# Kernel optimization log

Measured on AMD Instinct MI355X. Metric: run time of the kernel, lower is better.

Reference implementation:

```python
import jax, jax.numpy as jnp
import numpy as np

B, K, D = 256, 256, 3          # graphs, destroy sets per graph, destroy size
N_PER = 55                      # nodes per graph (from Linear(55+3, 1))
N = B * N_PER                   # total batched nodes
E = N * 8                       # edges, avg degree 8
EMB = 64


def setup_inputs() -> dict:
    key = jax.random.key(0)
    ks = jax.random.split(key, 16)
    inp = {
        'coords': jax.random.uniform(ks[0], (N, 2), dtype=jnp.float32),
        'src': jax.random.randint(ks[1], (E,), 0, N, dtype=jnp.int32),
        'dst': jax.random.randint(ks[2], (E,), 0, N, dtype=jnp.int32),
        'destroy_ids': jax.random.randint(ks[3], (B, K, D), 0, N_PER, dtype=jnp.int32),
        'W_embed': jax.random.normal(ks[4], (2, EMB), dtype=jnp.float32) * 0.5,
        'b_embed': jax.random.normal(ks[5], (EMB,), dtype=jnp.float32) * 0.1,
        'Wself': jax.random.normal(ks[6], (3, EMB, EMB), dtype=jnp.float32) * (1.0 / np.sqrt(EMB)),
        'Wneigh': jax.random.normal(ks[7], (3, EMB, EMB), dtype=jnp.float32) * (1.0 / np.sqrt(EMB)) * 0.1,
        'gnn_b': jax.random.normal(ks[8], (3, EMB), dtype=jnp.float32) * 0.1,
        'W1': jax.random.normal(ks[9], (EMB, 32), dtype=jnp.float32) * (1.0 / np.sqrt(EMB)),
        'b1': jax.random.normal(ks[10], (32,), dtype=jnp.float32) * 0.1,
        'W2': jax.random.normal(ks[11], (32, 32), dtype=jnp.float32) * (1.0 / np.sqrt(32)),
        'b2': jax.random.normal(ks[12], (32,), dtype=jnp.float32) * 0.1,
        'W3': jax.random.normal(ks[13], (32, 1), dtype=jnp.float32) * (1.0 / np.sqrt(32)),
        'b3': jax.random.normal(ks[14], (1,), dtype=jnp.float32) * 0.1,
        'Wp': jax.random.normal(ks[15], (N_PER + D, 1), dtype=jnp.float32) * (1.0 / np.sqrt(N_PER + D)),
        'bp': jnp.zeros((1,), dtype=jnp.float32),
    }
    return inp


def reference(coords, src, dst, destroy_ids, W_embed, b_embed, Wself, Wneigh,
              gnn_b, W1, b1, W2, b2, W3, b3, Wp, bp):
    lrelu = lambda x: jax.nn.leaky_relu(x, 0.01)
    # node coord embedding: [N, 64]
    h = coords @ W_embed + b_embed
    # residual message passing (GNN), 3 layers
    for l in range(Wself.shape[0]):
        agg = jax.ops.segment_sum(h[src], dst, num_segments=N)  # irregular gather/scatter
        h = jax.nn.relu(h @ Wself[l] + agg @ Wneigh[l] + gnn_b[l]) + h
    g_embed = h.reshape(B, N_PER, EMB)                 # [B, 55, 64]
    # vectorized replacement of the per-id .item() gather loops
    coords_b = coords.reshape(B, N_PER, 2)
    d_coords = jax.vmap(lambda c, idx: c[idx])(coords_b, destroy_ids)  # [B, K, 3, 2]
    d_embed = d_coords @ W_embed + b_embed             # [B, K, 3, 64]
    # concat graph embedding with each destroy-set embedding along node dim
    g_b = jnp.broadcast_to(g_embed[:, None], (B, K, N_PER, EMB))
    final = jnp.concatenate([g_b, d_embed], axis=2)    # [B, K, 58, 64]
    # MLP: 64->32->32->1 then pred over node dim 58->1
    x = lrelu(final @ W1 + b1)
    x = lrelu(x @ W2 + b2)
    x = (x @ W3 + b3)[..., 0]                          # [B, K, 58]
    out = (x @ Wp + bp)[..., 0]                        # [B, K]
    return out
```

## Files before the change

kernel.cpp:

```cpp
#include <hip/hip_runtime.h>
#include <hip/hip_bf16.h>

constexpr int NB   = 256;
constexpr int KK   = 256;
constexpr int NPER = 55;
constexpr int NN   = NB * NPER;
constexpr int EMB  = 64;
constexpr int CAP  = 32;
constexpr int NT   = 512;

using ull = unsigned long long;
__device__ __forceinline__ void st_f1(float* p, float x) {
  union { float f; unsigned u; } v; v.f = x;
  __hip_atomic_store((unsigned*)p, v.u, __ATOMIC_RELAXED, __HIP_MEMORY_SCOPE_AGENT);
}
__device__ __forceinline__ void st_f2(float* p, float x, float y) {
  union { float f[2]; ull u; } v; v.f[0] = x; v.f[1] = y;
  __hip_atomic_store((ull*)p, v.u, __ATOMIC_RELAXED, __HIP_MEMORY_SCOPE_AGENT);
}
__device__ __forceinline__ float2 ld_f2(const float* p) {
  union { ull u; float f[2]; } v;
  v.u = __hip_atomic_load((const ull*)p, __ATOMIC_RELAXED, __HIP_MEMORY_SCOPE_AGENT);
  return make_float2(v.f[0], v.f[1]);
}
__device__ __forceinline__ int ld_i1(const int* p) {
  return __hip_atomic_load(p, __ATOMIC_RELAXED, __HIP_MEMORY_SCOPE_AGENT);
}
__device__ __forceinline__ void st_i1(int* p, int x) {
  __hip_atomic_store(p, x, __ATOMIC_RELAXED, __HIP_MEMORY_SCOPE_AGENT);
}
__device__ __forceinline__ int2 ld_i2(const int* p) {
  union { ull u; int i[2]; } v;
  v.u = __hip_atomic_load((const ull*)p, __ATOMIC_RELAXED, __HIP_MEMORY_SCOPE_AGENT);
  return make_int2(v.i[0], v.i[1]);
}

constexpr int ZERO_N = NN + NB + 16;
__global__ __launch_bounds__(256) void init_kernel(int* __restrict__ p) {
  int i = blockIdx.x * 256 + threadIdx.x;
  if (i < ZERO_N) p[i] = 0;
}

__device__ __forceinline__ void grid_barrier(int* arr, int* flag, int ep) {
  __syncthreads();
  int tid = threadIdx.x;
  if (blockIdx.x == 0) {
    if (tid == 0) st_i1(&arr[0], ep);
    if (tid < NB) {
      while (ld_i1(&arr[tid]) < ep) __builtin_amdgcn_s_sleep(8);
    }
    __syncthreads();
    if (tid == 0) st_i1(flag, ep);
  } else {
    if (tid == 0) {
      st_i1(&arr[blockIdx.x], ep);
      while (ld_i1(flag) < ep) __builtin_amdgcn_s_sleep(8);
    }
  }
  __syncthreads();
}

__device__ __forceinline__ float mlp_lds(const float (&x)[64],
    const float* sW1, const float* sW2, const float* sW3,
    const float* sb1, const float* sb2, float b3v) {
  float a[32];
#pragma unroll
  for (int j = 0; j < 32; j++) a[j] = sb1[j];
#pragma unroll
  for (int i = 0; i < 64; i++) {
    float xi = x[i];
#pragma unroll
    for (int j = 0; j < 32; j++) a[j] = fmaf(xi, sW1[i * 32 + j], a[j]);
  }
#pragma unroll
  for (int j = 0; j < 32; j++) a[j] = (a[j] >= 0.f) ? a[j] : 0.01f * a[j];
  float c[32];
#pragma unroll
  for (int j = 0; j < 32; j++) c[j] = sb2[j];
#pragma unroll
  for (int i = 0; i < 32; i++) {
    float ai = a[i];
#pragma unroll
    for (int j = 0; j < 32; j++) c[j] = fmaf(ai, sW2[i * 32 + j], c[j]);
  }
#pragma unroll
  for (int j = 0; j < 32; j++) c[j] = (c[j] >= 0.f) ? c[j] : 0.01f * c[j];
  float r = b3v;
#pragma unroll
  for (int i = 0; i < 32; i++) r = fmaf(c[i], sW3[i], r);
  return r;
}

__global__ __launch_bounds__(NT) void mega_kernel(
    const float* __restrict__ coords, const int* __restrict__ src,
    const int* __restrict__ dst, const int* __restrict__ ids,
    const float* __restrict__ We, const float* __restrict__ be,
    const float* __restrict__ Wself, const float* __restrict__ Wneigh,
    const float* __restrict__ gnnb,
    const float* __restrict__ W1, const float* __restrict__ b1,
    const float* __restrict__ W2, const float* __restrict__ b2,
    const float* __restrict__ W3, const float* __restrict__ b3,
    const float* __restrict__ Wp, const float* __restrict__ bp,
    float* __restrict__ h0, float* __restrict__ h1,
    int* __restrict__ deg, int* __restrict__ bucket,
    int* __restrict__ arr, int* __restrict__ flag,
    float* __restrict__ out) {
  __shared__ __align__(16) float sWs[4096];
  __shared__ __align__(16) float sWn[4096];
  __shared__ __align__(16) float sh[NPER][EMB];
  __shared__ __align__(16) float uni[NPER * EMB];
  __shared__ int   sdeg[NPER];
  __shared__ float t_l[NPER];
  __shared__ float sWp[NPER + 3];
  __shared__ float sgsum, sbp_s;

  float (*sa)[EMB] = reinterpret_cast<float (*)[EMB]>(uni);
  int   (*sbk)[CAP] = reinterpret_cast<int (*)[CAP]>(uni);

  int tid = threadIdx.x;
  int b = blockIdx.x;
  int base = b * NPER;

  if (tid < NPER + 3) sWp[tid] = Wp[tid];
  if (tid == 0) sbp_s = bp[0];
  if (tid < 512)
    reinterpret_cast<float4*>(sWs)[tid] = reinterpret_cast<const float4*>(W1)[tid];
  if (tid < 256)
    reinterpret_cast<float4*>(sWs + 2048)[tid] = reinterpret_cast<const float4*>(W2)[tid];
  if (tid < 32) { sWn[tid] = W3[tid]; sWn[32 + tid] = b1[tid]; sWn[64 + tid] = b2[tid]; }
  if (tid == 0) sWn[96] = b3[0];
  if (tid < 8 * NPER) {
    int e = b * (8 * NPER) + tid;
    int d = dst[e];
    int s = src[e];
    int pos = atomicAdd(&deg[d], 1);
    if (pos < CAP) st_i1(&bucket[d * CAP + pos], s);
  }
  __syncthreads();

  if (tid < NPER) {
    int n = base + tid;
    float cx = coords[n * 2], cy = coords[n * 2 + 1];
    float x[64];
#pragma unroll
    for (int i = 0; i < 64; i++)
      x[i] = fmaf(cx, We[i], fmaf(cy, We[64 + i], be[i]));
    float* hv = h0 + (size_t)n * 64;
#pragma unroll
    for (int i = 0; i < 32; i++) st_f2(hv + 2 * i, x[2 * i], x[2 * i + 1]);
#pragma unroll
    for (int i = 0; i < 64; i++) sh[tid][i] = x[i];
    t_l[tid] = mlp_lds(x, sWs, sWs + 2048, sWn, sWn + 32, sWn + 64, sWn[96]);
  }
  __syncthreads();

  {
    const float4* Wsv = reinterpret_cast<const float4*>(Wself);
    const float4* Wnv = reinterpret_cast<const float4*>(Wneigh);
    for (int i = tid; i < 1024; i += NT) {
      reinterpret_cast<float4*>(sWs)[i] = Wsv[i];
      reinterpret_cast<float4*>(sWn)[i] = Wnv[i];
    }
  }

  grid_barrier(arr, flag, 1);
  if (tid < NPER) sdeg[tid] = min(ld_i1(&deg[base + tid]), CAP);

  for (int l = 0; l < 3; l++) {
    const float* hin  = (l == 1) ? h1 : h0;
    float*       hout = (l == 0) ? h1 : h0;
    const float* gbl = gnnb + l * 64;

    if (l == 0) {
      for (int i = tid; i < NPER * CAP / 2; i += NT) {
        int2 v = ld_i2(bucket + (size_t)base * CAP + 2 * i);
        sbk[0][2 * i] = v.x; sbk[0][2 * i + 1] = v.y;
      }
      __syncthreads();
    }

    int r = tid >> 3, o = tid & 7;
    float a0 = 0.f, a1 = 0.f, a2 = 0.f, a3 = 0.f;
    float a4 = 0.f, a5 = 0.f, a6 = 0.f, a7 = 0.f;
    if (r < NPER) {
      int dg = sdeg[r];
      size_t oo = (size_t)o * 8;
      for (int e0 = 0; e0 < dg; e0 += 2) {
        bool ok1 = (e0 + 1 < dg);
        int s0 = sbk[r][e0];
        int s1 = ok1 ? sbk[r][e0 + 1] : s0;
        const float* p0 = hin + (size_t)s0 * 64 + oo;
        const float* p1 = hin + (size_t)s1 * 64 + oo;
        float2 u0 = ld_f2(p0), u1 = ld_f2(p0 + 2), u2 = ld_f2(p0 + 4), u3 = ld_f2(p0 + 6);
        float2 w0 = ld_f2(p1), w1 = ld_f2(p1 + 2), w2 = ld_f2(p1 + 4), w3 = ld_f2(p1 + 6);
        a0 += u0.x; a1 += u0.y; a2 += u1.x; a3 += u1.y;
        a4 += u2.x; a5 += u2.y; a6 += u3.x; a7 += u3.y;
        if (ok1) {
          a0 += w0.x; a1 += w0.y; a2 += w1.x; a3 += w1.y;
          a4 += w2.x; a5 += w2.y; a6 += w3.x; a7 += w3.y;
        }
      }
    }
    __syncthreads();
    if (r < NPER) {
      float4* sap = reinterpret_cast<float4*>(&sa[r][o * 8]);
      sap[0] = make_float4(a0, a1, a2, a3);
      sap[1] = make_float4(a4, a5, a6, a7);
    }
    __syncthreads();

    int j = tid & 63;
    int g = tid >> 6;
    int nrows = (g < 7) ? 7 : 6;
    int rbase = g * 7;
    float bj = gbl[j];
    float acc[7];
#pragma unroll
    for (int nn = 0; nn < 7; nn++) acc[nn] = bj;
#pragma unroll
    for (int c = 0; c < 16; c++) {
      int ib = c * 4;
      float w0 = sWs[(ib + 0) * 64 + j], w1 = sWs[(ib + 1) * 64 + j];
      float w2 = sWs[(ib + 2) * 64 + j], w3 = sWs[(ib + 3) * 64 + j];
      float v0 = sWn[(ib + 0) * 64 + j], v1 = sWn[(ib + 1) * 64 + j];
      float v2 = sWn[(ib + 2) * 64 + j], v3 = sWn[(ib + 3) * 64 + j];
#pragma unroll
      for (int nn = 0; nn < 7; nn++) {
        if (nn < nrows) {
          int rr = rbase + nn;
          float4 hs = *reinterpret_cast<const float4*>(&sh[rr][ib]);
          float4 as = *reinterpret_cast<const float4*>(&sa[rr][ib]);
          float t = acc[nn];
          t = fmaf(hs.x, w0, t); t = fmaf(hs.y, w1, t);
          t = fmaf(hs.z, w2, t); t = fmaf(hs.w, w3, t);
          t = fmaf(as.x, v0, t); t = fmaf(as.y, v1, t);
          t = fmaf(as.z, v2, t); t = fmaf(as.w, v3, t);
          acc[nn] = t;
        }
      }
    }
    float res[7];
#pragma unroll
    for (int nn = 0; nn < 7; nn++) {
      if (nn < nrows) {
        int rr = rbase + nn;
        res[nn] = ((acc[nn] > 0.f) ? acc[nn] : 0.f) + sh[rr][j];
        if (l != 2) st_f1(&hout[(size_t)(base + rr) * 64 + j], res[nn]);
      }
    }
    __syncthreads();
#pragma unroll
    for (int nn = 0; nn < 7; nn++)
      if (nn < nrows) sh[rbase + nn][j] = res[nn];
    __syncthreads();

    if (l < 2) {
      for (int i = tid; i < NPER * CAP / 2; i += NT) {
        int2 v = ld_i2(bucket + (size_t)base * CAP + 2 * i);
        sbk[0][2 * i] = v.x; sbk[0][2 * i + 1] = v.y;
      }
      const float4* Wsv = reinterpret_cast<const float4*>(Wself + (l + 1) * 4096);
      const float4* Wnv = reinterpret_cast<const float4*>(Wneigh + (l + 1) * 4096);
      for (int i = tid; i < 1024; i += NT) {
        reinterpret_cast<float4*>(sWs)[i] = Wsv[i];
        reinterpret_cast<float4*>(sWn)[i] = Wnv[i];
      }
      grid_barrier(arr, flag, l + 2);
    }
  }

  if (tid < 512)
    reinterpret_cast<float4*>(sWs)[tid] = reinterpret_cast<const float4*>(W1)[tid];
  if (tid < 256)
    reinterpret_cast<float4*>(sWs + 2048)[tid] = reinterpret_cast<const float4*>(W2)[tid];
  if (tid < 32) { sWn[tid] = W3[tid]; sWn[32 + tid] = b1[tid]; sWn[64 + tid] = b2[tid]; }
  if (tid == 0) sWn[96] = b3[0];
  __syncthreads();

  if (tid < 64) {
    float v = 0.f;
    if (tid < NPER) {
      float x[64];
#pragma unroll
      for (int i = 0; i < 64; i++) x[i] = sh[tid][i];
      float rr = mlp_lds(x, sWs, sWs + 2048, sWn, sWn + 32, sWn + 64, sWn[96]);
      v = rr * sWp[tid];
    }
#pragma unroll
    for (int off = 32; off > 0; off >>= 1) v += __shfl_down(v, off, 64);
    if (tid == 0) sgsum = v;
  }
  __syncthreads();

  if (tid < KK) {
    const int* id = ids + ((size_t)b * KK + tid) * 3;
    int i0 = id[0], i1 = id[1], i2 = id[2];
    float o = sgsum + sbp_s;
    o = fmaf(t_l[i0], sWp[NPER + 0], o);
    o = fmaf(t_l[i1], sWp[NPER + 1], o);
    o = fmaf(t_l[i2], sWp[NPER + 2], o);
    out[(size_t)b * KK + tid] = o;
  }
}

extern "C" void kernel_launch(void* const* d_in, const int* in_sizes, int n_in,
                              void* d_out, int out_size, void* d_ws, size_t ws_size,
                              hipStream_t stream) {
  const float* coords = (const float*)d_in[0];
  const int*   src    = (const int*)d_in[1];
  const int*   dst    = (const int*)d_in[2];
  const int*   ids    = (const int*)d_in[3];
  const float* We     = (const float*)d_in[4];
  const float* be     = (const float*)d_in[5];
  const float* Wself  = (const float*)d_in[6];
  const float* Wneigh = (const float*)d_in[7];
  const float* gb     = (const float*)d_in[8];
  const float* W1     = (const float*)d_in[9];
  const float* b1     = (const float*)d_in[10];
  const float* W2     = (const float*)d_in[11];
  const float* b2     = (const float*)d_in[12];
  const float* W3     = (const float*)d_in[13];
  const float* b3     = (const float*)d_in[14];
  const float* Wp     = (const float*)d_in[15];
  const float* bp     = (const float*)d_in[16];
  float* out = (float*)d_out;

  float* ws = (float*)d_ws;
  float* h0 = ws;
  float* h1 = h0 + (size_t)NN * EMB;
  int* deg    = (int*)(h1 + (size_t)NN * EMB);
  int* arr    = deg + NN;
  int* flag   = arr + NB;
  int* bucket = flag + 16;

  init_kernel<<<(ZERO_N + 255) / 256, 256, 0, stream>>>(deg);
  mega_kernel<<<NB, NT, 0, stream>>>(
      coords, src, dst, ids, We, be, Wself, Wneigh, gb,
      W1, b1, W2, b2, W3, b3, Wp, bp,
      h0, h1, deg, bucket, arr, flag, out);
}
```

Before: 172.7 us.

## Parallelize per-node MLP across block, use plain vector loads, triple-buffer h

```diff
diff --git a/kernel.cpp b/kernel.cpp
--- a/kernel.cpp
+++ b/kernel.cpp
@@ -18,21 +18,11 @@
   union { float f[2]; ull u; } v; v.f[0] = x; v.f[1] = y;
   __hip_atomic_store((ull*)p, v.u, __ATOMIC_RELAXED, __HIP_MEMORY_SCOPE_AGENT);
 }
-__device__ __forceinline__ float2 ld_f2(const float* p) {
-  union { ull u; float f[2]; } v;
-  v.u = __hip_atomic_load((const ull*)p, __ATOMIC_RELAXED, __HIP_MEMORY_SCOPE_AGENT);
-  return make_float2(v.f[0], v.f[1]);
+__device__ __forceinline__ void st_i1(int* p, int x) {
+  __hip_atomic_store(p, x, __ATOMIC_RELAXED, __HIP_MEMORY_SCOPE_AGENT);
 }
 __device__ __forceinline__ int ld_i1(const int* p) {
   return __hip_atomic_load(p, __ATOMIC_RELAXED, __HIP_MEMORY_SCOPE_AGENT);
-}
-__device__ __forceinline__ void st_i1(int* p, int x) {
-  __hip_atomic_store(p, x, __ATOMIC_RELAXED, __HIP_MEMORY_SCOPE_AGENT);
-}
-__device__ __forceinline__ int2 ld_i2(const int* p) {
-  union { ull u; int i[2]; } v;
-  v.u = __hip_atomic_load((const ull*)p, __ATOMIC_RELAXED, __HIP_MEMORY_SCOPE_AGENT);
-  return make_int2(v.i[0], v.i[1]);
 }
 
 constexpr int ZERO_N = NN + NB + 16;
@@ -57,38 +47,38 @@
       while (ld_i1(flag) < ep) __builtin_amdgcn_s_sleep(8);
     }
   }
-  __syncthreads();
-}
-
-__device__ __forceinline__ float mlp_lds(const float (&x)[64],
-    const float* sW1, const float* sW2, const float* sW3,
-    const float* sb1, const float* sb2, float b3v) {
-  float a[32];
-#pragma unroll
-  for (int j = 0; j < 32; j++) a[j] = sb1[j];
-#pragma unroll
-  for (int i = 0; i < 64; i++) {
-    float xi = x[i];
-#pragma unroll
-    for (int j = 0; j < 32; j++) a[j] = fmaf(xi, sW1[i * 32 + j], a[j]);
-  }
-#pragma unroll
-  for (int j = 0; j < 32; j++) a[j] = (a[j] >= 0.f) ? a[j] : 0.01f * a[j];
-  float c[32];
-#pragma unroll
-  for (int j = 0; j < 32; j++) c[j] = sb2[j];
-#pragma unroll
-  for (int i = 0; i < 32; i++) {
-    float ai = a[i];
-#pragma unroll
-    for (int j = 0; j < 32; j++) c[j] = fmaf(ai, sW2[i * 32 + j], c[j]);
-  }
-#pragma unroll
-  for (int j = 0; j < 32; j++) c[j] = (c[j] >= 0.f) ? c[j] : 0.01f * c[j];
-  float r = b3v;
-#pragma unroll
-  for (int i = 0; i < 32; i++) r = fmaf(c[i], sW3[i], r);
-  return r;
+  __atomic_signal_fence(__ATOMIC_SEQ_CST);
+  __syncthreads();
+}
+
+__device__ __forceinline__ void mlp_all(const float (&sh)[NPER][EMB],
+    float* scr, const float* sW1, const float* sW2, const float* sW3,
+    const float* sb1, const float* sb2, float b3v, float* res, int tid) {
+  int grp = tid >> 5;
+  int u   = tid & 31;
+#pragma unroll
+  for (int pass = 0; pass < 4; pass++) {
+    int node = pass * 16 + grp;
+    if (node < NPER) {
+      float a = sb1[u];
+#pragma unroll
+      for (int i = 0; i < 64; i++) a = fmaf(sh[node][i], sW1[i * 32 + u], a);
+      a = (a >= 0.f) ? a : 0.01f * a;
+      scr[grp * 32 + u] = a;
+    }
+    __syncthreads();
+    if (node < NPER) {
+      float c = sb2[u];
+#pragma unroll
+      for (int i = 0; i < 32; i++) c = fmaf(scr[grp * 32 + i], sW2[i * 32 + u], c);
+      c = (c >= 0.f) ? c : 0.01f * c;
+      float v = c * sW3[u];
+#pragma unroll
+      for (int off = 16; off > 0; off >>= 1) v += __shfl_xor(v, off, 32);
+      if (u == 0) res[node] = v + b3v;
+    }
+    __syncthreads();
+  }
 }
 
 __global__ __launch_bounds__(NT) void mega_kernel(
@@ -101,7 +91,7 @@
     const float* __restrict__ W2, const float* __restrict__ b2,
     const float* __restrict__ W3, const float* __restrict__ b3,
     const float* __restrict__ Wp, const float* __restrict__ bp,
-    float* __restrict__ h0, float* __restrict__ h1,
+    float* __restrict__ h0, float* __restrict__ h1, float* __restrict__ h2,
     int* __restrict__ deg, int* __restrict__ bucket,
     int* __restrict__ arr, int* __restrict__ flag,
     float* __restrict__ out) {
@@ -111,10 +101,11 @@
   __shared__ __align__(16) float uni[NPER * EMB];
   __shared__ int   sdeg[NPER];
   __shared__ float t_l[NPER];
+  __shared__ float s_arr[NPER];
   __shared__ float sWp[NPER + 3];
   __shared__ float sgsum, sbp_s;
 
-  float (*sa)[EMB] = reinterpret_cast<float (*)[EMB]>(uni);
+  float (*sa)[EMB]  = reinterpret_cast<float (*)[EMB]>(uni);
   int   (*sbk)[CAP] = reinterpret_cast<int (*)[CAP]>(uni);
 
   int tid = threadIdx.x;
@@ -136,7 +127,6 @@
     int pos = atomicAdd(&deg[d], 1);
     if (pos < CAP) st_i1(&bucket[d * CAP + pos], s);
   }
-  __syncthreads();
 
   if (tid < NPER) {
     int n = base + tid;
@@ -150,9 +140,10 @@
     for (int i = 0; i < 32; i++) st_f2(hv + 2 * i, x[2 * i], x[2 * i + 1]);
 #pragma unroll
     for (int i = 0; i < 64; i++) sh[tid][i] = x[i];
-    t_l[tid] = mlp_lds(x, sWs, sWs + 2048, sWn, sWn + 32, sWn + 64, sWn[96]);
-  }
-  __syncthreads();
+  }
+  __syncthreads();
+
+  mlp_all(sh, uni, sWs, sWs + 2048, sWn, sWn + 32, sWn + 64, sWn[96], t_l, tid);
 
   {
     const float4* Wsv = reinterpret_cast<const float4*>(Wself);
@@ -164,18 +155,17 @@
   }
 
   grid_barrier(arr, flag, 1);
-  if (tid < NPER) sdeg[tid] = min(ld_i1(&deg[base + tid]), CAP);
+  if (tid < NPER) sdeg[tid] = min(deg[base + tid], CAP);
 
   for (int l = 0; l < 3; l++) {
-    const float* hin  = (l == 1) ? h1 : h0;
-    float*       hout = (l == 0) ? h1 : h0;
+    const float* hin  = (l == 0) ? h0 : (l == 1) ? h1 : h2;
+    float*       hout = (l == 0) ? h1 : h2;
     const float* gbl = gnnb + l * 64;
 
     if (l == 0) {
-      for (int i = tid; i < NPER * CAP / 2; i += NT) {
-        int2 v = ld_i2(bucket + (size_t)base * CAP + 2 * i);
-        sbk[0][2 * i] = v.x; sbk[0][2 * i + 1] = v.y;
-      }
+      for (int i = tid; i < NPER * CAP / 4; i += NT)
+        reinterpret_cast<int4*>(uni)[i] =
+            reinterpret_cast<const int4*>(bucket + (size_t)base * CAP)[i];
       __syncthreads();
     }
 
@@ -189,15 +179,15 @@
         bool ok1 = (e0 + 1 < dg);
         int s0 = sbk[r][e0];
         int s1 = ok1 ? sbk[r][e0 + 1] : s0;
-        const float* p0 = hin + (size_t)s0 * 64 + oo;
-        const float* p1 = hin + (size_t)s1 * 64 + oo;
-        float2 u0 = ld_f2(p0), u1 = ld_f2(p0 + 2), u2 = ld_f2(p0 + 4), u3 = ld_f2(p0 + 6);
-        float2 w0 = ld_f2(p1), w1 = ld_f2(p1 + 2), w2 = ld_f2(p1 + 4), w3 = ld_f2(p1 + 6);
-        a0 += u0.x; a1 += u0.y; a2 += u1.x; a3 += u1.y;
-        a4 += u2.x; a5 += u2.y; a6 += u3.x; a7 += u3.y;
+        const float4* p0 = reinterpret_cast<const float4*>(hin + (size_t)s0 * 64 + oo);
+        const float4* p1 = reinterpret_cast<const float4*>(hin + (size_t)s1 * 64 + oo);
+        float4 u0 = p0[0], u1 = p0[1];
+        float4 w0 = p1[0], w1 = p1[1];
+        a0 += u0.x; a1 += u0.y; a2 += u0.z; a3 += u0.w;
+        a4 += u1.x; a5 += u1.y; a6 += u1.z; a7 += u1.w;
         if (ok1) {
-          a0 += w0.x; a1 += w0.y; a2 += w1.x; a3 += w1.y;
-          a4 += w2.x; a5 += w2.y; a6 += w3.x; a7 += w3.y;
+          a0 += w0.x; a1 += w0.y; a2 += w0.z; a3 += w0.w;
+          a4 += w1.x; a5 += w1.y; a6 += w1.z; a7 += w1.w;
         }
       }
     }
@@ -255,10 +245,9 @@
     __syncthreads();
 
     if (l < 2) {
-      for (int i = tid; i < NPER * CAP / 2; i += NT) {
-        int2 v = ld_i2(bucket + (size_t)base * CAP + 2 * i);
-        sbk[0][2 * i] = v.x; sbk[0][2 * i + 1] = v.y;
-      }
+      for (int i = tid; i < NPER * CAP / 4; i += NT)
+        reinterpret_cast<int4*>(uni)[i] =
+            reinterpret_cast<const int4*>(bucket + (size_t)base * CAP)[i];
       const float4* Wsv = reinterpret_cast<const float4*>(Wself + (l + 1) * 4096);
       const float4* Wnv = reinterpret_cast<const float4*>(Wneigh + (l + 1) * 4096);
       for (int i = tid; i < 1024; i += NT) {
@@ -277,15 +266,10 @@
   if (tid == 0) sWn[96] = b3[0];
   __syncthreads();
 
+  mlp_all(sh, uni, sWs, sWs + 2048, sWn, sWn + 32, sWn + 64, sWn[96], s_arr, tid);
+
   if (tid < 64) {
-    float v = 0.f;
-    if (tid < NPER) {
-      float x[64];
-#pragma unroll
-      for (int i = 0; i < 64; i++) x[i] = sh[tid][i];
-      float rr = mlp_lds(x, sWs, sWs + 2048, sWn, sWn + 32, sWn + 64, sWn[96]);
-      v = rr * sWp[tid];
-    }
+    float v = (tid < NPER) ? s_arr[tid] * sWp[tid] : 0.f;
 #pragma unroll
     for (int off = 32; off > 0; off >>= 1) v += __shfl_down(v, off, 64);
     if (tid == 0) sgsum = v;
@@ -328,7 +312,8 @@
   float* ws = (float*)d_ws;
   float* h0 = ws;
   float* h1 = h0 + (size_t)NN * EMB;
-  int* deg    = (int*)(h1 + (size_t)NN * EMB);
+  float* h2 = h1 + (size_t)NN * EMB;
+  int* deg    = (int*)(h2 + (size_t)NN * EMB);
   int* arr    = deg + NN;
   int* flag   = arr + NB;
   int* bucket = flag + 16;
@@ -337,5 +322,5 @@
   mega_kernel<<<NB, NT, 0, stream>>>(
       coords, src, dst, ids, We, be, Wself, Wneigh, gb,
       W1, b1, W2, b2, W3, b3, Wp, bp,
-      h0, h1, deg, bucket, arr, flag, out);
-}
+      h0, h1, h2, deg, bucket, arr, flag, out);
+}
```

Result: faster. 159.8 us (-7.5%).
